# Kernel optimization log

Measured on AMD Instinct MI355X. Metric: run time of the kernel, lower is better.

The kernel has to match this reference:

```python
import jax, jax.numpy as jnp
from jax import lax
import numpy as np

VOCAB = 50000
HID = 512
BATCH = 64
T = 1000
N_ENT = 550


def setup_inputs() -> dict:
    key = jax.random.key(0)
    ks = jax.random.split(key, 9)
    inputs = jax.random.randint(ks[0], (BATCH, T), 0, VOCAB, dtype=jnp.int32)
    input_length = jnp.clip(jax.random.randint(ks[1], (BATCH,), 0, T, dtype=jnp.int32), 1, T)
    s = 1.0 / np.sqrt(HID)
    emb = jax.random.normal(ks[2], (VOCAB, HID), jnp.float32) * 0.05
    # per-layer LSTM kernels: input dim == HID for both layers (layer0 fed by embedding)
    W0 = jax.random.normal(ks[3], (2 * HID, 4 * HID), jnp.float32) * s
    b0 = jnp.zeros((4 * HID,), jnp.float32)
    W1 = jax.random.normal(ks[4], (2 * HID, 4 * HID), jnp.float32) * s
    b1 = jnp.zeros((4 * HID,), jnp.float32)
    W_out = jax.random.normal(ks[5], (HID, N_ENT), jnp.float32) * s
    b_out = jax.random.normal(ks[6], (N_ENT,), jnp.float32) * 0.02
    return {"inputs": inputs, "input_length": input_length, "emb": emb,
            "W0": W0, "b0": b0, "W1": W1, "b1": b1,
            "W_out": W_out, "b_out": b_out}


def _lstm_layer(x, W, b, lengths):
    """x: [B,T,D]; TF LSTMCell gate order i,j,f,o; forget_bias=0.0.
    dynamic_rnn semantics: past sequence_length, state is held and output zeroed."""
    B, Tn, _ = x.shape
    H = W.shape[1] // 4
    c0 = jnp.zeros((B, H), x.dtype)
    h0 = jnp.zeros((B, H), x.dtype)

    def step(carry, xt_t):
        c, h = carry
        xt, t = xt_t
        gates = jnp.concatenate([xt, h], axis=-1) @ W + b  # [B,4H]
        i, j, f, o = jnp.split(gates, 4, axis=-1)
        c_new = jax.nn.sigmoid(f) * c + jax.nn.sigmoid(i) * jnp.tanh(j)
        h_new = jax.nn.sigmoid(o) * jnp.tanh(c_new)
        m = (t < lengths)[:, None]
        c_out = jnp.where(m, c_new, c)
        h_out = jnp.where(m, h_new, h)
        y = jnp.where(m, h_new, jnp.zeros_like(h_new))
        return (c_out, h_out), y

    xs = (jnp.swapaxes(x, 0, 1), jnp.arange(Tn))
    _, ys = lax.scan(step, (c0, h0), xs)
    return jnp.swapaxes(ys, 0, 1)  # [B,T,H]


def reference(inputs, input_length, emb, W0, b0, W1, b1, W_out, b_out):
    x = emb[inputs]                              # [B,T,H] embedding lookup
    h1 = _lstm_layer(x, W0, b0, input_length)    # stacked layer 0
    h2 = _lstm_layer(h1, W1, b1, input_length)   # stacked layer 1
    last = h2[jnp.arange(h2.shape[0]), input_length - 1]  # [B,H] output at t=len-1
    logits = last @ W_out + b_out                # [B, n_entities]
    return logits
```

## Files before the change

kernel.cpp:

```cpp
#include <hip/hip_runtime.h>
#include <cstdint>
#include <cstddef>

#define HID   512
#define NB    64
#define SEQT  1000
#define NENT  550

#define NWG   256
#define NTHR  256
#define SLICES 128
#define KTOT  1024
#define KCH   128
#define NCH   8
#define IP    132

typedef unsigned long long ull;

__device__ __forceinline__ float sigm(float x) {
  x = fminf(fmaxf(x, -30.f), 30.f);
  return 1.f / (1.f + __expf(-x));
}
__device__ __forceinline__ float tanh_f(float x) {
  x = fminf(fmaxf(x, -15.f), 15.f);
  float e = __expf(2.f * x);
  return (e - 1.f) / (e + 1.f);
}
__device__ __forceinline__ void st_llc(float* p, float v) {
  __hip_atomic_store(p, v, __ATOMIC_RELAXED, __HIP_MEMORY_SCOPE_AGENT);
}
__device__ __forceinline__ ull ld_llc8(const float* p) {
  return __hip_atomic_load((const ull*)p, __ATOMIC_RELAXED, __HIP_MEMORY_SCOPE_AGENT);
}
__device__ __forceinline__ float ld_llc4(const float* p) {
  return __hip_atomic_load(p, __ATOMIC_RELAXED, __HIP_MEMORY_SCOPE_AGENT);
}

__global__ void __launch_bounds__(256)
pack_w(const float* __restrict__ W0, const float* __restrict__ W1,
       float4* __restrict__ Wp)
{
  const unsigned idx = blockIdx.x * 256u + threadIdx.x;
  const int g  = idx & 3;
  const int k  = (idx >> 2) & (KTOT - 1);
  const int sl = (idx >> 12) & (SLICES - 1);
  const int L  = idx >> 19;
  const float* W = L ? W1 : W0;
  Wp[idx] = *(const float4*)(W + (size_t)k * 2048 + g * HID + sl * 4);
}

__global__ void __launch_bounds__(NTHR, 1)
lstm_persistent(const int* __restrict__ tok, const int* __restrict__ len,
                const float* __restrict__ emb,
                const float* __restrict__ W0, const float* __restrict__ b0,
                const float* __restrict__ W1, const float* __restrict__ b1,
                const float* __restrict__ Wout, const float* __restrict__ bout,
                float* __restrict__ out, unsigned char* __restrict__ ws,
                const float4* __restrict__ Wp, int packed)
{
  __shared__ float4 Wl[KTOT * 4];
  __shared__ float inl[2][NB][IP];
  __shared__ float gl[NB][16];
  __shared__ float bl[16];
  __shared__ int   s_maxlen;

  const int tid = threadIdx.x;
  const int wg  = blockIdx.x;
  const int L   = wg >> 7;
  const int sl  = wg & (SLICES - 1);

  unsigned* cnt = (unsigned*)ws;
  float* h0b   = (float*)(ws + 256);
  float* h1b   = h0b + 2 * NB * HID;
  float* y0b   = h1b + 2 * NB * HID;
  float* lastb = y0b + 2 * NB * HID;

  const float* Wsrc = L ? W1 : W0;
  const float* bsrc = L ? b1 : b0;

  const int b   = tid & 63;
  const int seg = tid >> 6;
  const int ub  = tid >> 2;
  const int uu  = tid & 3;
  const int gu  = sl * 4 + uu;

  if (tid < 16) bl[tid] = bsrc[(tid >> 2) * HID + sl * 4 + (tid & 3)];
  if (tid < 64) {
    int l = len[tid];
    #pragma unroll
    for (int off = 32; off; off >>= 1) l = max(l, __shfl_xor(l, off));
    if (tid == 0) s_maxlen = l;
  }
  const int len_b  = len[b];
  const int len_ub = len[ub];

  if (packed) {
    const float4* wsrc = Wp + (size_t)(L * SLICES + sl) * KTOT * 4;
    #pragma unroll 4
    for (int i = tid; i < KTOT * 4; i += NTHR)
      Wl[i] = wsrc[i];
  } else {
    for (int i = tid; i < KTOT * 4; i += NTHR) {
      const int k = i >> 2, g = i & 3;
      Wl[i] = *(const float4*)(Wsrc + (size_t)k * 2048 + g * HID + sl * 4);
    }
  }
  __syncthreads();
  const int maxlen = s_maxlen;

  float c_st = 0.f, h_st = 0.f;
  unsigned target = 0;

  for (int r = 0; r <= maxlen; ++r) {
    const bool active = (L == 0) ? (r < maxlen) : (r >= 1);
    if (active) {
      const int t = (L == 0) ? r : (r - 1);
      const bool aliveS = (t < len_b);

      const float* hprev = (L ? h1b : h0b) + ((r + 1) & 1) * NB * HID + b * HID;
      const float* xsrc  = (L == 0)
          ? (emb + (size_t)tok[b * SEQT + t] * HID)
          : (y0b + ((r + 1) & 1) * NB * HID + b * HID);

      ull v[16];
      auto stage = [&](int c) {
        if (!aliveS) return;
        const float* src = ((c < 4) ? (xsrc + c * KCH) : (hprev + (c - 4) * KCH)) + seg * 32;
        if (c < 4 && L == 0) {
          #pragma unroll
          for (int i = 0; i < 16; ++i) v[i] = *(const ull*)(src + 2 * i);
        } else {
          #pragma unroll
          for (int i = 0; i < 16; ++i) v[i] = ld_llc8(src + 2 * i);
        }
      };
      auto wr = [&](int c) {
        if (!aliveS) return;
        float* dst = &inl[c & 1][b][seg * 32];
        #pragma unroll
        for (int i = 0; i < 16; ++i) *(ull*)(dst + 2 * i) = v[i];
      };

      float a0 = 0.f, a1 = 0.f, a2 = 0.f, a3 = 0.f;
      auto comp = [&](int c) {
        const float* row = &inl[c & 1][b][0];
        const float4* wb = Wl + (size_t)c * KCH * 4 + seg;
        #pragma unroll 4
        for (int k = 0; k < KCH; k += 4) {
          const float4 iv = *(const float4*)(row + k);
          const float4 w0 = wb[(k + 0) * 4];
          const float4 w1 = wb[(k + 1) * 4];
          const float4 w2 = wb[(k + 2) * 4];
          const float4 w3 = wb[(k + 3) * 4];
          a0 = fmaf(iv.x, w0.x, a0); a1 = fmaf(iv.x, w0.y, a1);
          a2 = fmaf(iv.x, w0.z, a2); a3 = fmaf(iv.x, w0.w, a3);
          a0 = fmaf(iv.y, w1.x, a0); a1 = fmaf(iv.y, w1.y, a1);
          a2 = fmaf(iv.y, w1.z, a2); a3 = fmaf(iv.y, w1.w, a3);
          a0 = fmaf(iv.z, w2.x, a0); a1 = fmaf(iv.z, w2.y, a1);
          a2 = fmaf(iv.z, w2.z, a2); a3 = fmaf(iv.z, w2.w, a3);
          a0 = fmaf(iv.w, w3.x, a0); a1 = fmaf(iv.w, w3.y, a1);
          a2 = fmaf(iv.w, w3.z, a2); a3 = fmaf(iv.w, w3.w, a3);
        }
      };

      stage(0);
      wr(0);
      __syncthreads();
      for (int c = 0; c < NCH; ++c) {
        if (c < NCH - 1) stage(c + 1);
        comp(c);
        if (c < NCH - 1) wr(c + 1);
        __syncthreads();
      }

      *(float4*)&gl[b][seg << 2] = make_float4(a0, a1, a2, a3);
      __syncthreads();

      const bool alive = (t < len_ub);
      float gi = gl[ub][uu]      + bl[uu];
      float gj = gl[ub][4 + uu]  + bl[4 + uu];
      float gf = gl[ub][8 + uu]  + bl[8 + uu];
      float go = gl[ub][12 + uu] + bl[12 + uu];
      float cn = sigm(gf) * c_st + sigm(gi) * tanh_f(gj);
      float hn = sigm(go) * tanh_f(cn);
      if (alive) { c_st = cn; h_st = hn; }
      float* hb = (L ? h1b : h0b) + (r & 1) * NB * HID;
      st_llc(&hb[ub * HID + gu], h_st);
      if (L == 0) {
        st_llc(&y0b[(r & 1) * NB * HID + ub * HID + gu], alive ? hn : 0.f);
      } else if (t == len_ub - 1) {
        st_llc(&lastb[ub * HID + gu], hn);
      }
      __syncthreads();
    }

    target += NWG;
    asm volatile("s_waitcnt vmcnt(0) lgkmcnt(0)" ::: "memory");
    __syncthreads();
    if (tid == 0) {
      __hip_atomic_fetch_add(cnt, 1u, __ATOMIC_RELAXED, __HIP_MEMORY_SCOPE_AGENT);
      while (__hip_atomic_load(cnt, __ATOMIC_RELAXED, __HIP_MEMORY_SCOPE_AGENT) < target)
        __builtin_amdgcn_s_sleep(4);
    }
    __syncthreads();
  }

  const int go_ = wg * NTHR + tid;
  if (go_ < NB * NENT) {
    const int bb = go_ / NENT;
    const int e  = go_ - bb * NENT;
    const float* lrow = lastb + bb * HID;
    float s = bout[e];
    #pragma unroll 8
    for (int k = 0; k < HID; ++k)
      s = fmaf(ld_llc4(lrow + k), Wout[k * NENT + e], s);
    out[go_] = s;
  }
}

extern "C" void kernel_launch(void* const* d_in, const int* in_sizes, int n_in,
                              void* d_out, int out_size, void* d_ws, size_t ws_size,
                              hipStream_t stream) {
  (void)in_sizes; (void)n_in; (void)out_size;
  const int*   tok  = (const int*)d_in[0];
  const int*   len  = (const int*)d_in[1];
  const float* emb  = (const float*)d_in[2];
  const float* W0   = (const float*)d_in[3];
  const float* b0   = (const float*)d_in[4];
  const float* W1   = (const float*)d_in[5];
  const float* b1   = (const float*)d_in[6];
  const float* Wout = (const float*)d_in[7];
  const float* bout = (const float*)d_in[8];
  float* out = (float*)d_out;
  unsigned char* ws = (unsigned char*)d_ws;

  const size_t zbytes   = 256 + (size_t)7 * NB * HID * sizeof(float);
  const size_t pack_off = (zbytes + 255) & ~(size_t)255;
  const size_t pack_sz  = (size_t)2 * SLICES * KTOT * 4 * sizeof(float4);
  const int    packed   = (ws_size >= pack_off + pack_sz) ? 1 : 0;
  float4* Wp = (float4*)(ws + pack_off);

  hipMemsetAsync(ws, 0, zbytes, stream);
  if (packed) {
    const int n4 = 2 * SLICES * KTOT * 4;
    pack_w<<<n4 / 256, 256, 0, stream>>>(W0, W1, Wp);
  }

  void* args[] = {(void*)&tok, (void*)&len, (void*)&emb, (void*)&W0, (void*)&b0,
                  (void*)&W1, (void*)&b1, (void*)&Wout, (void*)&bout,
                  (void*)&out, (void*)&ws, (void*)&Wp, (void*)&packed};
  hipLaunchCooperativeKernel((const void*)lstm_persistent, dim3(NWG), dim3(NTHR),
                             args, 0, stream);
}
```

Before: 31.79 ms.

## Register-tile the per-step LSTM gate GEMM with wave-local input staging

Each thread now computes a 4-batch by 4-column outer-product tile of gate partial sums instead of one batch row against four columns. The LDS input buffer is laid out so each wavefront stages and reads only its own K segment, which lets the per-chunk block barriers go. Weights are repacked column-major with padding, and partial sums are reduced across segments through a padded LDS buffer. The spin-wait sleep is shortened. The per-batch skip of loads for finished sequences is removed, so dead batches are now fetched too.

```diff
diff --git a/kernel.cpp b/kernel.cpp
--- a/kernel.cpp
+++ b/kernel.cpp
@@ -12,10 +12,11 @@
 #define SLICES 128
 #define KTOT  1024
 #define KCH   128
-#define NCH   8
-#define IP    132
+#define WP    1028
+#define GP    68
 
 typedef unsigned long long ull;
+typedef float f32x4 __attribute__((ext_vector_type(4)));
 
 __device__ __forceinline__ float sigm(float x) {
   x = fminf(fmaxf(x, -30.f), 30.f);
@@ -38,15 +39,15 @@
 
 __global__ void __launch_bounds__(256)
 pack_w(const float* __restrict__ W0, const float* __restrict__ W1,
-       float4* __restrict__ Wp)
+       float* __restrict__ Wp)
 {
   const unsigned idx = blockIdx.x * 256u + threadIdx.x;
-  const int g  = idx & 3;
-  const int k  = (idx >> 2) & (KTOT - 1);
-  const int sl = (idx >> 12) & (SLICES - 1);
-  const int L  = idx >> 19;
+  const int k   = idx & (KTOT - 1);
+  const int col = (idx >> 10) & 15;
+  const int sl  = (idx >> 14) & (SLICES - 1);
+  const int L   = idx >> 21;
   const float* W = L ? W1 : W0;
-  Wp[idx] = *(const float4*)(W + (size_t)k * 2048 + g * HID + sl * 4);
+  Wp[idx] = W[(size_t)k * 2048 + (col >> 2) * HID + sl * 4 + (col & 3)];
 }
 
 __global__ void __launch_bounds__(NTHR, 1)
@@ -56,11 +57,11 @@
                 const float* __restrict__ W1, const float* __restrict__ b1,
                 const float* __restrict__ Wout, const float* __restrict__ bout,
                 float* __restrict__ out, unsigned char* __restrict__ ws,
-                const float4* __restrict__ Wp, int packed)
+                const float* __restrict__ Wp, int packed)
 {
-  __shared__ float4 Wl[KTOT * 4];
-  __shared__ float inl[2][NB][IP];
-  __shared__ float gl[NB][16];
+  __shared__ float Wl2[16 * WP];
+  __shared__ float inl2[2][4][8][64][4];
+  __shared__ float glp[NB * GP];
   __shared__ float bl[16];
   __shared__ int   s_maxlen;
 
@@ -80,6 +81,8 @@
 
   const int b   = tid & 63;
   const int seg = tid >> 6;
+  const int bq  = tid & 15;
+  const int cq  = (tid >> 4) & 3;
   const int ub  = tid >> 2;
   const int uu  = tid & 3;
   const int gu  = sl * 4 + uu;
@@ -91,18 +94,19 @@
     for (int off = 32; off; off >>= 1) l = max(l, __shfl_xor(l, off));
     if (tid == 0) s_maxlen = l;
   }
-  const int len_b  = len[b];
   const int len_ub = len[ub];
 
   if (packed) {
-    const float4* wsrc = Wp + (size_t)(L * SLICES + sl) * KTOT * 4;
-    #pragma unroll 4
-    for (int i = tid; i < KTOT * 4; i += NTHR)
-      Wl[i] = wsrc[i];
+    const float* wsrc = Wp + (size_t)(L * SLICES + sl) * (16 * KTOT);
+    for (int i = tid * 4; i < 16 * KTOT; i += NTHR * 4) {
+      const int col = i >> 10, k = i & (KTOT - 1);
+      *(float4*)&Wl2[col * WP + k] = *(const float4*)(wsrc + i);
+    }
   } else {
-    for (int i = tid; i < KTOT * 4; i += NTHR) {
-      const int k = i >> 2, g = i & 3;
-      Wl[i] = *(const float4*)(Wsrc + (size_t)k * 2048 + g * HID + sl * 4);
+    for (int i = tid; i < 16 * KTOT; i += NTHR) {
+      const int col = i >> 10, k = i & (KTOT - 1);
+      Wl2[col * WP + k] =
+          Wsrc[(size_t)k * 2048 + (col >> 2) * HID + sl * 4 + (col & 3)];
     }
   }
   __syncthreads();
@@ -115,17 +119,56 @@
     const bool active = (L == 0) ? (r < maxlen) : (r >= 1);
     if (active) {
       const int t = (L == 0) ? r : (r - 1);
-      const bool aliveS = (t < len_b);
 
       const float* hprev = (L ? h1b : h0b) + ((r + 1) & 1) * NB * HID + b * HID;
       const float* xsrc  = (L == 0)
           ? (emb + (size_t)tok[b * SEQT + t] * HID)
           : (y0b + ((r + 1) & 1) * NB * HID + b * HID);
 
-      ull v[16];
-      auto stage = [&](int c) {
-        if (!aliveS) return;
-        const float* src = ((c < 4) ? (xsrc + c * KCH) : (hprev + (c - 4) * KCH)) + seg * 32;
+      float acc[4][4] = {};
+      auto comp = [&](int c) {
+        const float (*ivb)[64][4] = inl2[c & 1][seg];
+        const int k0 = c * KCH + seg * 32;
+        const float* w0 = &Wl2[(0 * 4 + cq) * WP + k0];
+        const float* w1 = &Wl2[(1 * 4 + cq) * WP + k0];
+        const float* w2 = &Wl2[(2 * 4 + cq) * WP + k0];
+        const float* w3 = &Wl2[(3 * 4 + cq) * WP + k0];
+        #pragma unroll
+        for (int jj = 0; jj < 8; ++jj) {
+          const f32x4 x0 = *(const f32x4*)ivb[jj][bq +  0];
+          const f32x4 x1 = *(const f32x4*)ivb[jj][bq + 16];
+          const f32x4 x2 = *(const f32x4*)ivb[jj][bq + 32];
+          const f32x4 x3 = *(const f32x4*)ivb[jj][bq + 48];
+          const f32x4 g0 = *(const f32x4*)(w0 + jj * 4);
+          const f32x4 g1 = *(const f32x4*)(w1 + jj * 4);
+          const f32x4 g2 = *(const f32x4*)(w2 + jj * 4);
+          const f32x4 g3 = *(const f32x4*)(w3 + jj * 4);
+          #pragma unroll
+          for (int e = 0; e < 4; ++e) {
+            acc[0][0] = fmaf(x0[e], g0[e], acc[0][0]);
+            acc[0][1] = fmaf(x0[e], g1[e], acc[0][1]);
+            acc[0][2] = fmaf(x0[e], g2[e], acc[0][2]);
+            acc[0][3] = fmaf(x0[e], g3[e], acc[0][3]);
+            acc[1][0] = fmaf(x1[e], g0[e], acc[1][0]);
+            acc[1][1] = fmaf(x1[e], g1[e], acc[1][1]);
+            acc[1][2] = fmaf(x1[e], g2[e], acc[1][2]);
+            acc[1][3] = fmaf(x1[e], g3[e], acc[1][3]);
+            acc[2][0] = fmaf(x2[e], g0[e], acc[2][0]);
+            acc[2][1] = fmaf(x2[e], g1[e], acc[2][1]);
+            acc[2][2] = fmaf(x2[e], g2[e], acc[2][2]);
+            acc[2][3] = fmaf(x2[e], g3[e], acc[2][3]);
+            acc[3][0] = fmaf(x3[e], g0[e], acc[3][0]);
+            acc[3][1] = fmaf(x3[e], g1[e], acc[3][1]);
+            acc[3][2] = fmaf(x3[e], g2[e], acc[3][2]);
+            acc[3][3] = fmaf(x3[e], g3[e], acc[3][3]);
+          }
+        }
+      };
+
+      for (int c = 0; c < 8; ++c) {
+        const float* src =
+            ((c < 4) ? (xsrc + c * KCH) : (hprev + (c - 4) * KCH)) + seg * 32;
+        ull v[16];
         if (c < 4 && L == 0) {
           #pragma unroll
           for (int i = 0; i < 16; ++i) v[i] = *(const ull*)(src + 2 * i);
@@ -133,54 +176,32 @@
           #pragma unroll
           for (int i = 0; i < 16; ++i) v[i] = ld_llc8(src + 2 * i);
         }
-      };
-      auto wr = [&](int c) {
-        if (!aliveS) return;
-        float* dst = &inl[c & 1][b][seg * 32];
+        float (*dstb)[64][4] = inl2[c & 1][seg];
         #pragma unroll
-        for (int i = 0; i < 16; ++i) *(ull*)(dst + 2 * i) = v[i];
-      };
-
-      float a0 = 0.f, a1 = 0.f, a2 = 0.f, a3 = 0.f;
-      auto comp = [&](int c) {
-        const float* row = &inl[c & 1][b][0];
-        const float4* wb = Wl + (size_t)c * KCH * 4 + seg;
-        #pragma unroll 4
-        for (int k = 0; k < KCH; k += 4) {
-          const float4 iv = *(const float4*)(row + k);
-          const float4 w0 = wb[(k + 0) * 4];
-          const float4 w1 = wb[(k + 1) * 4];
-          const float4 w2 = wb[(k + 2) * 4];
-          const float4 w3 = wb[(k + 3) * 4];
-          a0 = fmaf(iv.x, w0.x, a0); a1 = fmaf(iv.x, w0.y, a1);
-          a2 = fmaf(iv.x, w0.z, a2); a3 = fmaf(iv.x, w0.w, a3);
-          a0 = fmaf(iv.y, w1.x, a0); a1 = fmaf(iv.y, w1.y, a1);
-          a2 = fmaf(iv.y, w1.z, a2); a3 = fmaf(iv.y, w1.w, a3);
-          a0 = fmaf(iv.z, w2.x, a0); a1 = fmaf(iv.z, w2.y, a1);
-          a2 = fmaf(iv.z, w2.z, a2); a3 = fmaf(iv.z, w2.w, a3);
-          a0 = fmaf(iv.w, w3.x, a0); a1 = fmaf(iv.w, w3.y, a1);
-          a2 = fmaf(iv.w, w3.z, a2); a3 = fmaf(iv.w, w3.w, a3);
+        for (int jj = 0; jj < 8; ++jj) {
+          *(ull*)&dstb[jj][b][0] = v[2 * jj];
+          *(ull*)&dstb[jj][b][2] = v[2 * jj + 1];
         }
-      };
-
-      stage(0);
-      wr(0);
+        comp(c);
+      }
+
+      #pragma unroll
+      for (int mb = 0; mb < 4; ++mb)
+        #pragma unroll
+        for (int g = 0; g < 4; ++g)
+          glp[(bq + 16 * mb) * GP + cq * 16 + g * 4 + seg] = acc[mb][g];
       __syncthreads();
-      for (int c = 0; c < NCH; ++c) {
-        if (c < NCH - 1) stage(c + 1);
-        comp(c);
-        if (c < NCH - 1) wr(c + 1);
-        __syncthreads();
-      }
-
-      *(float4*)&gl[b][seg << 2] = make_float4(a0, a1, a2, a3);
-      __syncthreads();
-
+
+      const float* gp = &glp[ub * GP + uu * 16];
+      const f32x4 q0 = *(const f32x4*)(gp + 0);
+      const f32x4 q1 = *(const f32x4*)(gp + 4);
+      const f32x4 q2 = *(const f32x4*)(gp + 8);
+      const f32x4 q3 = *(const f32x4*)(gp + 12);
       const bool alive = (t < len_ub);
-      float gi = gl[ub][uu]      + bl[uu];
-      float gj = gl[ub][4 + uu]  + bl[4 + uu];
-      float gf = gl[ub][8 + uu]  + bl[8 + uu];
-      float go = gl[ub][12 + uu] + bl[12 + uu];
+      float gi = (q0[0] + q0[1]) + (q0[2] + q0[3]) + bl[uu];
+      float gj = (q1[0] + q1[1]) + (q1[2] + q1[3]) + bl[4 + uu];
+      float gf = (q2[0] + q2[1]) + (q2[2] + q2[3]) + bl[8 + uu];
+      float go = (q3[0] + q3[1]) + (q3[2] + q3[3]) + bl[12 + uu];
       float cn = sigm(gf) * c_st + sigm(gi) * tanh_f(gj);
       float hn = sigm(go) * tanh_f(cn);
       if (alive) { c_st = cn; h_st = hn; }
@@ -191,7 +212,6 @@
       } else if (t == len_ub - 1) {
         st_llc(&lastb[ub * HID + gu], hn);
       }
-      __syncthreads();
     }
 
     target += NWG;
@@ -200,7 +220,7 @@
     if (tid == 0) {
       __hip_atomic_fetch_add(cnt, 1u, __ATOMIC_RELAXED, __HIP_MEMORY_SCOPE_AGENT);
       while (__hip_atomic_load(cnt, __ATOMIC_RELAXED, __HIP_MEMORY_SCOPE_AGENT) < target)
-        __builtin_amdgcn_s_sleep(4);
+        __builtin_amdgcn_s_sleep(1);
     }
     __syncthreads();
   }
@@ -236,14 +256,14 @@
 
   const size_t zbytes   = 256 + (size_t)7 * NB * HID * sizeof(float);
   const size_t pack_off = (zbytes + 255) & ~(size_t)255;
-  const size_t pack_sz  = (size_t)2 * SLICES * KTOT * 4 * sizeof(float4);
+  const size_t pack_sz  = (size_t)2 * SLICES * 16 * KTOT * sizeof(float);
   const int    packed   = (ws_size >= pack_off + pack_sz) ? 1 : 0;
-  float4* Wp = (float4*)(ws + pack_off);
+  float* Wp = (float*)(ws + pack_off);
 
   hipMemsetAsync(ws, 0, zbytes, stream);
   if (packed) {
-    const int n4 = 2 * SLICES * KTOT * 4;
-    pack_w<<<n4 / 256, 256, 0, stream>>>(W0, W1, Wp);
+    const int n = 2 * SLICES * 16 * KTOT;
+    pack_w<<<n / 256, 256, 0, stream>>>(W0, W1, Wp);
   }
 
   void* args[] = {(void*)&tok, (void*)&len, (void*)&emb, (void*)&W0, (void*)&b0,
```

New measurement: 34.21 ms. +7.6%, slower.
